# Optimization experiments

Measured on AMD Instinct MI355X. Metric: run time of the kernel, lower is better.

## Reference

```python
import jax, jax.numpy as jnp
import numpy as np

N_NODES = 50000
N_EDGES = 800000
IN_CH, HID_CH, OUT_CH = 128, 128, 64


def setup_inputs() -> dict:
    key = jax.random.key(0)
    ks = jax.random.split(key, 8)
    x = jax.random.normal(ks[0], (N_NODES, IN_CH), dtype=jnp.float32)
    edge_index = jax.random.randint(ks[1], (2, N_EDGES), 0, N_NODES, dtype=jnp.int64)
    # PyG SAGEConv params: lin_l (applied to aggregated neighbors, has bias),
    # lin_r (applied to root node, no bias). Stored here as [in, out] matrices.
    s1 = 1.0 / np.sqrt(IN_CH)
    s2 = 1.0 / np.sqrt(HID_CH)
    W1l = jax.random.uniform(ks[2], (IN_CH, HID_CH), jnp.float32, -s1, s1)
    b1 = jnp.zeros((HID_CH,), jnp.float32)
    W1r = jax.random.uniform(ks[3], (IN_CH, HID_CH), jnp.float32, -s1, s1)
    W2l = jax.random.uniform(ks[4], (HID_CH, OUT_CH), jnp.float32, -s2, s2)
    b2 = jnp.zeros((OUT_CH,), jnp.float32)
    W2r = jax.random.uniform(ks[5], (HID_CH, OUT_CH), jnp.float32, -s2, s2)
    return {"x": x, "edge_index": edge_index, "W1l": W1l, "b1": b1,
            "W1r": W1r, "W2l": W2l, "b2": b2, "W2r": W2r}


def _sage_conv(x, src, dst, Wl, b, Wr):
    # mean-aggregate source features onto targets, then linear transform
    msg = x[src]                                        # [E, d] gather
    agg = jax.ops.segment_sum(msg, dst, num_segments=N_NODES)   # [N, d]
    deg = jax.ops.segment_sum(jnp.ones((src.shape[0],), x.dtype), dst,
                              num_segments=N_NODES)     # [N]
    mean = agg / jnp.maximum(deg, 1.0)[:, None]
    return mean @ Wl + b + x @ Wr


def reference(x, edge_index, W1l, b1, W1r, W2l, b2, W2r):
    src, dst = edge_index[0], edge_index[1]
    h = jax.nn.relu(_sage_conv(x, src, dst, W1l, b1, W1r))
    # F.dropout(p=0.3) is identity in eval mode
    return _sage_conv(h, src, dst, W2l, b2, W2r)
```

## Files before the change

### kernel.cpp

```cpp
#include <hip/hip_runtime.h>
#include <hip/hip_bf16.h>


#define TBLOCK 256
#define MAXBUCK 256
#define HGRID 512

typedef __attribute__((ext_vector_type(8))) short short8;
typedef __attribute__((ext_vector_type(4))) float f32x4;

__device__ __forceinline__ float bf2f(ushort u) {
    union { unsigned int i; float f; } v;
    v.i = (unsigned int)u << 16;
    return v.f;
}
__device__ __forceinline__ ushort f2bf(float f) {
    union { float f; unsigned int u; } v;
    v.f = f;
    unsigned int r = v.u + 0x7fffu + ((v.u >> 16) & 1u);
    return (ushort)(r >> 16);
}

__device__ __forceinline__ int block_detect_is64(const int* __restrict__ edges) {
    __shared__ int sbad[4];
    int tid = threadIdx.x;
    int bad = 0;
    for (int i = tid; i < 2048; i += TBLOCK)
        if (edges[2 * i + 1] != 0) bad = 1;
    unsigned long long b = __ballot(bad);
    if ((tid & 63) == 0) sbad[tid >> 6] = (b != 0) ? 1 : 0;
    __syncthreads();
    int flag = (sbad[0] | sbad[1] | sbad[2] | sbad[3]) ? 0 : 1;
    __syncthreads();
    return flag;
}

__device__ __forceinline__ int load_src(const int* e, long long i, int E, int is64) {
    return is64 ? e[2 * i] : e[i];
}
__device__ __forceinline__ int load_dst(const int* e, long long i, int E, int is64) {
    return is64 ? e[2 * (long long)E + 2 * i] : e[(long long)E + i];
}

__device__ __forceinline__ void scan_total(const int* __restrict__ total, int NBUCK,
                                           int* __restrict__ s) {
    int t = threadIdx.x;
    s[t] = (t < NBUCK) ? total[t] : 0;
    __syncthreads();
    for (int off = 1; off < TBLOCK; off <<= 1) {
        int xv = (t >= off) ? s[t - off] : 0;
        __syncthreads();
        s[t] += xv;
        __syncthreads();
    }
}

__global__ __launch_bounds__(TBLOCK) void histprep_k(
    const float* __restrict__ x,
    const float* __restrict__ W1l, const float* __restrict__ W1r,
    const float* __restrict__ W2l, const float* __restrict__ W2r,
    const int* __restrict__ edges, int E, int NBUCK,
    ushort* __restrict__ xb, ushort* __restrict__ wc1, ushort* __restrict__ wc2,
    int* __restrict__ counts, int n8, int nxb) {
    __shared__ int lh[MAXBUCK];
    const int b = blockIdx.x;
    const int t = threadIdx.x;
    if (b < HGRID) {
        const int is64 = block_detect_is64(edges);
        for (int i = t; i < NBUCK; i += TBLOCK) lh[i] = 0;
        __syncthreads();
        const int per = (E + HGRID - 1) / HGRID;
        const int b0 = b * per, b1 = min(E, b0 + per);
        for (int i = b0 + t; i < b1; i += TBLOCK)
            atomicAdd(&lh[load_dst(edges, i, E, is64) >> 8], 1);
        __syncthreads();
        for (int j = t; j < NBUCK; j += TBLOCK)
            counts[j * HGRID + b] = lh[j];
    } else {
        int pb = b - HGRID;
        if (pb < nxb) {
            int i = pb * TBLOCK + t;
            if (i >= n8) return;
            const float4* p = (const float4*)x + (size_t)i * 2;
            float4 a = p[0], bb = p[1];
            short8 o;
            o[0] = f2bf(a.x); o[1] = f2bf(a.y); o[2] = f2bf(a.z); o[3] = f2bf(a.w);
            o[4] = f2bf(bb.x); o[5] = f2bf(bb.y); o[6] = f2bf(bb.z); o[7] = f2bf(bb.w);
            *(short8*)(xb + (size_t)i * 8) = o;
        } else {
            int i = (pb - nxb) * TBLOCK + t;
            if (i < 32768) {
                int j = i & 7;
                int rest = i >> 3;
                int n = rest & 127;
                int k = ((rest >> 7) << 3) | j;
                float w = (k < 128) ? W1l[k * 128 + n] : W1r[(k - 128) * 128 + n];
                wc1[i] = f2bf(w);
            } else if (i < 49152) {
                int i2 = i - 32768;
                int j = i2 & 7;
                int rest = i2 >> 3;
                int n = rest & 127;
                int k = ((rest >> 7) << 3) | j;
                float w = (n < 64) ? W2l[k * 64 + n] : W2r[k * 64 + (n - 64)];
                wc2[i2] = f2bf(w);
            }
        }
    }
}

__global__ __launch_bounds__(TBLOCK) void scanA_k(int* __restrict__ counts,
                                                  int* __restrict__ total) {
    __shared__ int s[TBLOCK];
    const int j = blockIdx.x;
    const int t = threadIdx.x;
    int* row = counts + (size_t)j * HGRID;
    int v0 = row[2 * t];
    int v1 = row[2 * t + 1];
    s[t] = v0 + v1;
    __syncthreads();
    for (int off = 1; off < TBLOCK; off <<= 1) {
        int xv = (t >= off) ? s[t - off] : 0;
        __syncthreads();
        s[t] += xv;
        __syncthreads();
    }
    int excl = (t == 0) ? 0 : s[t - 1];
    row[2 * t] = excl;
    row[2 * t + 1] = excl + v0;
    if (t == TBLOCK - 1) total[j] = s[t];
}

__global__ __launch_bounds__(TBLOCK) void scatterA_k(const int* __restrict__ edges, int E,
                                                     const int* __restrict__ counts,
                                                     const int* __restrict__ total,
                                                     unsigned int* __restrict__ packed,
                                                     int NBUCK) {
    const int is64 = block_detect_is64(edges);
    __shared__ int s[TBLOCK];
    __shared__ int lb[MAXBUCK];
    __shared__ int lh[MAXBUCK];
    const int b = blockIdx.x;
    const int t = threadIdx.x;
    scan_total(total, NBUCK, s);
    if (t < NBUCK) {
        int excl = (t == 0) ? 0 : s[t - 1];
        lb[t] = excl + counts[t * HGRID + b];
        lh[t] = 0;
    }
    __syncthreads();
    const int per = (E + HGRID - 1) / HGRID;
    const int b0 = b * per, b1 = min(E, b0 + per);
    for (int i = b0 + t; i < b1; i += TBLOCK) {
        int sv = load_src(edges, i, E, is64);
        int d = load_dst(edges, i, E, is64);
        int bk = d >> 8;
        int pos = lb[bk] + atomicAdd(&lh[bk], 1);
        packed[pos] = (unsigned int)sv | ((unsigned int)(d & 255) << 24);
    }
}

__global__ __launch_bounds__(TBLOCK) void buildB_k(const unsigned int* __restrict__ packed,
                                                   const int* __restrict__ total,
                                                   int* __restrict__ offs,
                                                   int* __restrict__ degi,
                                                   float* __restrict__ invdeg,
                                                   int* __restrict__ csr, int N, int NBUCK) {
    __shared__ int s[TBLOCK];
    __shared__ int cnt[TBLOCK], scn[TBLOCK], cur[TBLOCK];
    int t = threadIdx.x;
    int bucket = blockIdx.x;
    scan_total(total, NBUCK, s);
    int e0 = (bucket == 0) ? 0 : s[bucket - 1];
    int e1 = s[bucket];
    cnt[t] = 0;
    cur[t] = 0;
    __syncthreads();
    for (int i = e0 + t; i < e1; i += TBLOCK)
        atomicAdd(&cnt[packed[i] >> 24], 1);
    __syncthreads();
    scn[t] = cnt[t];
    __syncthreads();
    for (int off = 1; off < TBLOCK; off <<= 1) {
        int x = (t >= off) ? scn[t - off] : 0;
        __syncthreads();
        scn[t] += x;
        __syncthreads();
    }
    int excl = (t == 0) ? 0 : scn[t - 1];
    int node = bucket * 256 + t;
    if (node < N) {
        offs[node] = e0 + excl;
        degi[node] = cnt[t];
        invdeg[node] = 1.0f / fmaxf((float)cnt[t], 1.0f);
    }
    __syncthreads();
    cnt[t] = excl;
    __syncthreads();
    for (int i = e0 + t; i < e1; i += TBLOCK) {
        unsigned int p = packed[i];
        int nl = p >> 24;
        int pos = e0 + cnt[nl] + atomicAdd(&cur[nl], 1);
        csr[pos] = (int)(p & 0xFFFFFFu);
    }
}

template <int C, bool ACCUM>
__global__ __launch_bounds__(TBLOCK) void gatherb_k(const ushort* __restrict__ feat,
                                                    const int* __restrict__ csr,
                                                    const int* __restrict__ offs,
                                                    const int* __restrict__ degi,
                                                    const float* __restrict__ invdeg,
                                                    ushort* __restrict__ outB,
                                                    float* __restrict__ outF, int N) {
    constexpr int G = C / 8;
    constexpr int NPB = TBLOCK / G;
    int n = blockIdx.x * NPB + threadIdx.x / G;
    if (n >= N) return;
    int lane = threadIdx.x % G;
    int c = lane * 8;
    int s0 = offs[n];
    int d = degi[n];
    float acc[8] = {0.f, 0.f, 0.f, 0.f, 0.f, 0.f, 0.f, 0.f};
    for (int base = 0; base < d; base += G) {
        int rem = d - base;
        int my = (lane < rem) ? csr[s0 + base + lane] : 0;
        if (rem >= G) {
#pragma unroll
            for (int j = 0; j < G; j++) {
                int s = __shfl(my, j, G);
                short8 v = *(const short8*)(feat + (size_t)s * C + c);
#pragma unroll
                for (int q = 0; q < 8; q++) acc[q] += bf2f((ushort)v[q]);
            }
        } else {
            for (int j = 0; j < rem; j++) {
                int s = __shfl(my, j, G);
                short8 v = *(const short8*)(feat + (size_t)s * C + c);
#pragma unroll
                for (int q = 0; q < 8; q++) acc[q] += bf2f((ushort)v[q]);
            }
        }
    }
    float sc = invdeg[n];
    if (ACCUM) {
        float* o = outF + (size_t)n * C + c;
        float4 p0 = *(float4*)o;
        float4 p1 = *(float4*)(o + 4);
        p0.x += sc * acc[0]; p0.y += sc * acc[1]; p0.z += sc * acc[2]; p0.w += sc * acc[3];
        p1.x += sc * acc[4]; p1.y += sc * acc[5]; p1.z += sc * acc[6]; p1.w += sc * acc[7];
        *(float4*)o = p0;
        *(float4*)(o + 4) = p1;
    } else {
        short8 o;
#pragma unroll
        for (int q = 0; q < 8; q++) o[q] = f2bf(sc * acc[q]);
        *(short8*)(outB + (size_t)n * C + c) = o;
    }
}

template <int KTOT, int EPI>
__global__ __launch_bounds__(TBLOCK) void gemm_k(const ushort* __restrict__ A0,
                                                 const ushort* __restrict__ A1,
                                                 const ushort* __restrict__ wc,
                                                 const float* __restrict__ bias,
                                                 ushort* __restrict__ outB,
                                                 float* __restrict__ outF, int N) {
    __shared__ __align__(16) ushort sW[KTOT * 128];
    for (int i = threadIdx.x * 8; i < KTOT * 128; i += TBLOCK * 8)
        *(short8*)&sW[i] = *(const short8*)&wc[i];
    __syncthreads();

    const int wave = threadIdx.x >> 6;
    const int lane = threadIdx.x & 63;
    const int quad = lane >> 4;
    const int l16 = lane & 15;
    const int m0 = (blockIdx.x * 4 + wave) * 32;
    if (m0 >= N) return;

    f32x4 acc[2][8];
#pragma unroll
    for (int t = 0; t < 2; t++)
#pragma unroll
        for (int nt = 0; nt < 8; nt++) acc[t][nt] = (f32x4){0.f, 0.f, 0.f, 0.f};

    const int k0q = quad * 8;
#pragma unroll
    for (int kb = 0; kb < KTOT; kb += 32) {
        int k = kb + k0q;
        const ushort* abase = (KTOT == 256 && k >= 128) ? (A1 + (k - 128)) : (A0 + k);
        short8 a[2];
#pragma unroll
        for (int t = 0; t < 2; t++) {
            int m = m0 + t * 16 + l16;
            if (m > N - 1) m = N - 1;
            a[t] = *(const short8*)(abase + (size_t)m * 128);
        }
#pragma unroll
        for (int nt = 0; nt < 8; nt++) {
            short8 b = *(const short8*)&sW[((k >> 3) * 128 + nt * 16 + l16) * 8];
            acc[0][nt] = __builtin_amdgcn_mfma_f32_16x16x32_bf16(a[0], b, acc[0][nt], 0, 0, 0);
            acc[1][nt] = __builtin_amdgcn_mfma_f32_16x16x32_bf16(a[1], b, acc[1][nt], 0, 0, 0);
        }
    }

#pragma unroll
    for (int t = 0; t < 2; t++) {
#pragma unroll
        for (int r = 0; r < 4; r++) {
            int m = m0 + t * 16 + quad * 4 + r;
            if (m >= N) continue;
#pragma unroll
            for (int nt = 0; nt < 8; nt++) {
                int n = nt * 16 + l16;
                float v = acc[t][nt][r];
                if (EPI == 1) {
                    v = fmaxf(v + bias[n], 0.f);
                    outB[(size_t)m * 128 + n] = f2bf(v);
                } else {
                    if (n < 64) outB[(size_t)m * 64 + n] = f2bf(v);
                    else outF[(size_t)m * 64 + (n - 64)] = v + bias[n - 64];
                }
            }
        }
    }
}

extern "C" void kernel_launch(void* const* d_in, const int* in_sizes, int n_in,
                              void* d_out, int out_size, void* d_ws, size_t ws_size,
                              hipStream_t stream) {
    const float* x = (const float*)d_in[0];
    const int* edges = (const int*)d_in[1];
    const float* W1l = (const float*)d_in[2];
    const float* b1 = (const float*)d_in[3];
    const float* W1r = (const float*)d_in[4];
    const float* W2l = (const float*)d_in[5];
    const float* b2 = (const float*)d_in[6];
    const float* W2r = (const float*)d_in[7];
    float* out = (float*)d_out;

    const int N = in_sizes[0] / 128;
    const int E = in_sizes[1] / 2;
    const int Na = (N + 63) & ~63;
    const int NBUCK = (N + 255) >> 8;
    const int n8 = N * 128 / 8;
    const int nxb = (n8 + TBLOCK - 1) / TBLOCK;

    char* WS = (char*)d_ws;
    size_t off = 0;
    auto alloc = [&](size_t bytes) {
        void* p = WS + off;
        off = (off + bytes + 255) & ~(size_t)255;
        return p;
    };
    int* counts = (int*)alloc((size_t)MAXBUCK * HGRID * 4);
    int* total = (int*)alloc((size_t)MAXBUCK * 4);
    int* offs = (int*)alloc((size_t)Na * 4);
    int* degi = (int*)alloc((size_t)Na * 4);
    float* invdeg = (float*)alloc((size_t)Na * 4);
    unsigned int* packed = (unsigned int*)alloc((size_t)E * 4);
    int* csr = (int*)alloc((size_t)E * 4);
    ushort* xb = (ushort*)alloc((size_t)N * 128 * 2);
    ushort* agg1b = (ushort*)alloc((size_t)N * 128 * 2);
    ushort* hb = (ushort*)alloc((size_t)N * 128 * 2);
    ushort* t2b = (ushort*)alloc((size_t)N * 64 * 2);
    ushort* wc1 = (ushort*)alloc(32768 * 2);
    ushort* wc2 = (ushort*)alloc(16384 * 2);

    histprep_k<<<HGRID + nxb + 192, TBLOCK, 0, stream>>>(
        x, W1l, W1r, W2l, W2r, edges, E, NBUCK, xb, wc1, wc2, counts, n8, nxb);
    scanA_k<<<NBUCK, TBLOCK, 0, stream>>>(counts, total);
    scatterA_k<<<HGRID, TBLOCK, 0, stream>>>(edges, E, counts, total, packed, NBUCK);
    buildB_k<<<NBUCK, TBLOCK, 0, stream>>>(packed, total, offs, degi, invdeg, csr, N, NBUCK);

    gatherb_k<128, false><<<(N + 15) / 16, TBLOCK, 0, stream>>>(
        xb, csr, offs, degi, invdeg, agg1b, nullptr, N);
    gemm_k<256, 1><<<(N + 127) / 128, TBLOCK, 0, stream>>>(
        agg1b, xb, wc1, b1, hb, nullptr, N);

    gemm_k<128, 2><<<(N + 127) / 128, TBLOCK, 0, stream>>>(
        hb, nullptr, wc2, b2, t2b, out, N);
    gatherb_k<64, true><<<(N + 31) / 32, TBLOCK, 0, stream>>>(
        t2b, csr, offs, degi, invdeg, nullptr, out, N);
}
```

Measured before the change: 194.4 us.

## Fuse layer-1 neighbor mean gather into the layer-1 MFMA GEMM kernel

Replaces the separate layer-1 gather kernel and GEMM with one kernel in which each lane gathers and averages neighbor rows for its assigned node directly into MFMA A-fragment registers. The GEMM then consumes them without the agg1b intermediate buffer. This removes a full N x 128 bf16 write and read plus one launch. In exchange, the gather now has one lane per node walking edges serially with 64-byte reads per row. That gives far less memory-level parallelism and more warp divergence from varying degrees than the previous dedicated gather. The 64KB LDS weight tile also limits occupancy during the latency-bound gather phase.

```diff
diff --git a/kernel.cpp b/kernel.cpp
--- a/kernel.cpp
+++ b/kernel.cpp
@@ -259,13 +259,116 @@
     }
 }
 
-template <int KTOT, int EPI>
-__global__ __launch_bounds__(TBLOCK) void gemm_k(const ushort* __restrict__ A0,
-                                                 const ushort* __restrict__ A1,
-                                                 const ushort* __restrict__ wc,
-                                                 const float* __restrict__ bias,
-                                                 ushort* __restrict__ outB,
-                                                 float* __restrict__ outF, int N) {
+__global__ __launch_bounds__(TBLOCK) void gg1_k(const ushort* __restrict__ xb,
+                                                const int* __restrict__ csr,
+                                                const int* __restrict__ offs,
+                                                const int* __restrict__ degi,
+                                                const float* __restrict__ invdeg,
+                                                const ushort* __restrict__ wc1,
+                                                const float* __restrict__ b1,
+                                                ushort* __restrict__ hb, int N) {
+    __shared__ __align__(16) ushort sW[256 * 128];
+    for (int i = threadIdx.x * 8; i < 256 * 128; i += TBLOCK * 8)
+        *(short8*)&sW[i] = *(const short8*)&wc1[i];
+
+    const int wave = threadIdx.x >> 6;
+    const int lane = threadIdx.x & 63;
+    const int quad = lane >> 4;
+    const int l16 = lane & 15;
+    const int m0 = blockIdx.x * 128 + wave * 32;
+    const int cq = quad * 8;
+
+    short8 aagg[2][4];
+#pragma unroll
+    for (int t = 0; t < 2; t++) {
+        int m = m0 + t * 16 + l16;
+        if (m > N - 1) m = N - 1;
+        int s0 = offs[m];
+        int d = degi[m];
+        float ga[4][8];
+#pragma unroll
+        for (int c = 0; c < 4; c++)
+#pragma unroll
+            for (int q = 0; q < 8; q++) ga[c][q] = 0.f;
+        for (int e = 0; e < d; e++) {
+            int s = csr[s0 + e];
+            const ushort* row = xb + (size_t)s * 128 + cq;
+            short8 v0 = *(const short8*)(row);
+            short8 v1 = *(const short8*)(row + 32);
+            short8 v2 = *(const short8*)(row + 64);
+            short8 v3 = *(const short8*)(row + 96);
+#pragma unroll
+            for (int q = 0; q < 8; q++) {
+                ga[0][q] += bf2f((ushort)v0[q]);
+                ga[1][q] += bf2f((ushort)v1[q]);
+                ga[2][q] += bf2f((ushort)v2[q]);
+                ga[3][q] += bf2f((ushort)v3[q]);
+            }
+        }
+        float iv = invdeg[m];
+#pragma unroll
+        for (int c = 0; c < 4; c++)
+#pragma unroll
+            for (int q = 0; q < 8; q++) aagg[t][c][q] = f2bf(ga[c][q] * iv);
+    }
+    __syncthreads();
+
+    f32x4 acc[2][8];
+#pragma unroll
+    for (int t = 0; t < 2; t++)
+#pragma unroll
+        for (int nt = 0; nt < 8; nt++) acc[t][nt] = (f32x4){0.f, 0.f, 0.f, 0.f};
+
+#pragma unroll
+    for (int kb = 0; kb < 128; kb += 32) {
+        int c = kb >> 5;
+        int k = kb + cq;
+#pragma unroll
+        for (int nt = 0; nt < 8; nt++) {
+            short8 b = *(const short8*)&sW[((k >> 3) * 128 + nt * 16 + l16) * 8];
+            acc[0][nt] = __builtin_amdgcn_mfma_f32_16x16x32_bf16(aagg[0][c], b, acc[0][nt], 0, 0, 0);
+            acc[1][nt] = __builtin_amdgcn_mfma_f32_16x16x32_bf16(aagg[1][c], b, acc[1][nt], 0, 0, 0);
+        }
+    }
+#pragma unroll
+    for (int kb = 128; kb < 256; kb += 32) {
+        int k = kb + cq;
+        short8 a[2];
+#pragma unroll
+        for (int t = 0; t < 2; t++) {
+            int m = m0 + t * 16 + l16;
+            if (m > N - 1) m = N - 1;
+            a[t] = *(const short8*)(xb + (size_t)m * 128 + (k - 128));
+        }
+#pragma unroll
+        for (int nt = 0; nt < 8; nt++) {
+            short8 b = *(const short8*)&sW[((k >> 3) * 128 + nt * 16 + l16) * 8];
+            acc[0][nt] = __builtin_amdgcn_mfma_f32_16x16x32_bf16(a[0], b, acc[0][nt], 0, 0, 0);
+            acc[1][nt] = __builtin_amdgcn_mfma_f32_16x16x32_bf16(a[1], b, acc[1][nt], 0, 0, 0);
+        }
+    }
+
+#pragma unroll
+    for (int t = 0; t < 2; t++)
+#pragma unroll
+        for (int r = 0; r < 4; r++) {
+            int m = m0 + t * 16 + quad * 4 + r;
+            if (m >= N) continue;
+#pragma unroll
+            for (int nt = 0; nt < 8; nt++) {
+                int n = nt * 16 + l16;
+                float v = fmaxf(acc[t][nt][r] + b1[n], 0.f);
+                hb[(size_t)m * 128 + n] = f2bf(v);
+            }
+        }
+}
+
+__global__ __launch_bounds__(TBLOCK) void gemm2_k(const ushort* __restrict__ A0,
+                                                  const ushort* __restrict__ wc,
+                                                  const float* __restrict__ bias,
+                                                  ushort* __restrict__ outB,
+                                                  float* __restrict__ outF, int N) {
+    constexpr int KTOT = 128;
     __shared__ __align__(16) ushort sW[KTOT * 128];
     for (int i = threadIdx.x * 8; i < KTOT * 128; i += TBLOCK * 8)
         *(short8*)&sW[i] = *(const short8*)&wc[i];
@@ -288,13 +391,12 @@
 #pragma unroll
     for (int kb = 0; kb < KTOT; kb += 32) {
         int k = kb + k0q;
-        const ushort* abase = (KTOT == 256 && k >= 128) ? (A1 + (k - 128)) : (A0 + k);
         short8 a[2];
 #pragma unroll
         for (int t = 0; t < 2; t++) {
             int m = m0 + t * 16 + l16;
             if (m > N - 1) m = N - 1;
-            a[t] = *(const short8*)(abase + (size_t)m * 128);
+            a[t] = *(const short8*)(A0 + (size_t)m * 128 + k);
         }
 #pragma unroll
         for (int nt = 0; nt < 8; nt++) {
@@ -314,13 +416,8 @@
             for (int nt = 0; nt < 8; nt++) {
                 int n = nt * 16 + l16;
                 float v = acc[t][nt][r];
-                if (EPI == 1) {
-                    v = fmaxf(v + bias[n], 0.f);
-                    outB[(size_t)m * 128 + n] = f2bf(v);
-                } else {
-                    if (n < 64) outB[(size_t)m * 64 + n] = f2bf(v);
-                    else outF[(size_t)m * 64 + (n - 64)] = v + bias[n - 64];
-                }
+                if (n < 64) outB[(size_t)m * 64 + n] = f2bf(v);
+                else outF[(size_t)m * 64 + (n - 64)] = v + bias[n - 64];
             }
         }
     }
@@ -361,7 +458,6 @@
     unsigned int* packed = (unsigned int*)alloc((size_t)E * 4);
     int* csr = (int*)alloc((size_t)E * 4);
     ushort* xb = (ushort*)alloc((size_t)N * 128 * 2);
-    ushort* agg1b = (ushort*)alloc((size_t)N * 128 * 2);
     ushort* hb = (ushort*)alloc((size_t)N * 128 * 2);
     ushort* t2b = (ushort*)alloc((size_t)N * 64 * 2);
     ushort* wc1 = (ushort*)alloc(32768 * 2);
@@ -373,13 +469,11 @@
     scatterA_k<<<HGRID, TBLOCK, 0, stream>>>(edges, E, counts, total, packed, NBUCK);
     buildB_k<<<NBUCK, TBLOCK, 0, stream>>>(packed, total, offs, degi, invdeg, csr, N, NBUCK);
 
-    gatherb_k<128, false><<<(N + 15) / 16, TBLOCK, 0, stream>>>(
-        xb, csr, offs, degi, invdeg, agg1b, nullptr, N);
-    gemm_k<256, 1><<<(N + 127) / 128, TBLOCK, 0, stream>>>(
-        agg1b, xb, wc1, b1, hb, nullptr, N);
-
-    gemm_k<128, 2><<<(N + 127) / 128, TBLOCK, 0, stream>>>(
-        hb, nullptr, wc2, b2, t2b, out, N);
+    gg1_k<<<(N + 127) / 128, TBLOCK, 0, stream>>>(
+        xb, csr, offs, degi, invdeg, wc1, b1, hb, N);
+
+    gemm2_k<<<(N + 127) / 128, TBLOCK, 0, stream>>>(
+        hb, wc2, b2, t2b, out, N);
     gatherb_k<64, true><<<(N + 31) / 32, TBLOCK, 0, stream>>>(
         t2b, csr, offs, degi, invdeg, nullptr, out, N);
 }
```

Measured after the change: 211.9 us. 9.0% more time.
